# Kernel tuning notes

Measured on AMD Instinct MI355X. Metric: run time of the kernel, lower is better.

## Reference

```python
import jax, jax.numpy as jnp
import numpy as np

L_MAX = 2    # l in {0,1,2}, m-dim sizes 2l+1
NU_MAX = 3   # body order
K = 8        # number of CG m-combinations kept per l_tuple
Q = 16       # radial channels
S = 256      # atomic environments (samples)


def _build_structure():
    """Deterministically build combine_indices + multiplicities (module state).
    Returns {nu: [(l_tuple, idx_prev[K], idx_1[K], mult[K]), ...]} in sorted order."""
    rng = np.random.default_rng(0)
    struct = {}
    # nu = 2: l_tuples are nondecreasing pairs; previous level is LE_1 with m-dim 2*l1+1
    struct[2] = []
    for l1 in range(L_MAX + 1):
        for l2 in range(l1, L_MAX + 1):
            ip = jnp.asarray(rng.integers(0, 2 * l1 + 1, K), dtype=jnp.int32)
            i1 = jnp.asarray(rng.integers(0, 2 * l2 + 1, K), dtype=jnp.int32)
            mult = jnp.asarray((rng.random(K) + 0.5).astype(np.float32))
            struct[2].append(((l1, l2), ip, i1, mult))
    # nu = 3: previous level tensors have m-dim K
    struct[3] = []
    for l1 in range(L_MAX + 1):
        for l2 in range(l1, L_MAX + 1):
            for l3 in range(l2, L_MAX + 1):
                ip = jnp.asarray(rng.integers(0, K, K), dtype=jnp.int32)
                i1 = jnp.asarray(rng.integers(0, 2 * l3 + 1, K), dtype=jnp.int32)
                mult = jnp.asarray((rng.random(K) + 0.5).astype(np.float32))
                struct[3].append(((l1, l2, l3), ip, i1, mult))
    return struct


def setup_inputs() -> dict:
    key = jax.random.key(0)
    k0, k1, k2 = jax.random.split(key, 3)
    return {
        "LE1_l0": jax.random.normal(k0, (1, Q, S), dtype=jnp.float32),
        "LE1_l1": jax.random.normal(k1, (3, Q, S), dtype=jnp.float32),
        "LE1_l2": jax.random.normal(k2, (5, Q, S), dtype=jnp.float32),
    }


def reference(LE1_l0, LE1_l1, LE1_l2):
    struct = _build_structure()
    LE1 = {(0,): LE1_l0, (1,): LE1_l1, (2,): LE1_l2}
    feats = {1: LE1}
    # Build all levels from UNSCALED parents (multiplicities applied afterwards,
    # matching the torch loop order exactly).
    for nu in range(2, NU_MAX + 1):
        cur = {}
        for lt, ip, i1, _ in struct[nu]:
            A = jnp.take(feats[nu - 1][lt[:-1]], ip, axis=0)[:, :, None, :]  # [K, F, 1, S]
            B = jnp.take(LE1[(lt[-1],)], i1, axis=0)[:, None, :, :]          # [K, 1, Q, S]
            cur[lt] = (A * B).reshape(K, -1, S)                               # [K, F*Q, S]
        feats[nu] = cur
    # Apply multiplicities, then flatten everything into one [total_rows, S] output
    outs = []
    for nu in range(2, NU_MAX + 1):
        for lt, _, _, mult in struct[nu]:
            outs.append((feats[nu][lt] * mult[:, None, None]).reshape(-1, S))
    return jnp.concatenate(outs, axis=0)
```

## Files before the change

### kernel.cpp

```cpp
#include <hip/hip_runtime.h>
#include <stdint.h>
#include <stddef.h>

#define KK 8
#define QQ 16
#define SS 256
#define NU2_ROWS 12288u

typedef float f32x4 __attribute__((ext_vector_type(4)));

namespace {

struct NpPcg64 {
  unsigned __int128 state, inc;
  uint32_t uinteger;
  bool has_uint32;

  static unsigned __int128 mul128() {
    return (((unsigned __int128)2549297995355413924ULL) << 64) | 4865540595714422341ULL;
  }
  void step() { state = state * mul128() + inc; }
  uint64_t next64() {
    step();
    uint64_t hi = (uint64_t)(state >> 64), lo = (uint64_t)state;
    uint64_t x = hi ^ lo;
    unsigned rot = (unsigned)(state >> 122) & 63u;
    return (x >> rot) | (x << ((64u - rot) & 63u));
  }
  uint32_t next32() {
    if (has_uint32) { has_uint32 = false; return uinteger; }
    uint64_t n = next64();
    has_uint32 = true;
    uinteger = (uint32_t)(n >> 32);
    return (uint32_t)n;
  }
  double nextd() {
    return (double)(next64() >> 11) * (1.0 / 9007199254740992.0);
  }
  uint32_t lemire32(uint32_t rng) {
    uint32_t excl = rng + 1u;
    uint64_t m = (uint64_t)next32() * (uint64_t)excl;
    uint32_t leftover = (uint32_t)m;
    if (leftover < excl) {
      uint32_t threshold = (uint32_t)((0xFFFFFFFFu - rng) % excl);
      while (leftover < threshold) {
        m = (uint64_t)next32() * (uint64_t)excl;
        leftover = (uint32_t)m;
      }
    }
    return (uint32_t)(m >> 32);
  }
  void integers(int high, int* out, int n) {
    if (high <= 1) { for (int i = 0; i < n; i++) out[i] = 0; return; }
    uint32_t rng = (uint32_t)(high - 1);
    for (int i = 0; i < n; i++) out[i] = (int)lemire32(rng);
  }
  void mults(float* out, int n) {
    for (int i = 0; i < n; i++) out[i] = (float)(nextd() + 0.5);
  }
};

void seed_rng0(NpPcg64& r) {
  uint32_t pool[4];
  uint32_t hc = 0x43b0d7e5u;
  auto hashmix = [&hc](uint32_t v) -> uint32_t {
    v ^= hc; hc *= 0x931e8875u; v *= hc; v ^= v >> 16; return v;
  };
  auto mix = [](uint32_t x, uint32_t y) -> uint32_t {
    uint32_t m = 0xca01f9ddu * x - 0x4973f715u * y; m ^= m >> 16; return m;
  };
  for (int i = 0; i < 4; i++) pool[i] = hashmix(0u);
  for (int is = 0; is < 4; is++)
    for (int id = 0; id < 4; id++)
      if (is != id) pool[id] = mix(pool[id], hashmix(pool[is]));
  uint32_t hb = 0x8b51f9ddu;
  uint32_t w[8];
  for (int i = 0; i < 8; i++) {
    uint32_t v = pool[i & 3];
    v ^= hb; hb *= 0x58f38dedu; v *= hb; v ^= v >> 16;
    w[i] = v;
  }
  uint64_t sd[4];
  for (int i = 0; i < 4; i++) sd[i] = (uint64_t)w[2 * i] | ((uint64_t)w[2 * i + 1] << 32);
  unsigned __int128 initstate = (((unsigned __int128)sd[0]) << 64) | sd[1];
  unsigned __int128 initseq   = (((unsigned __int128)sd[2]) << 64) | sd[3];
  r.state = 0; r.inc = (initseq << 1) | 1;
  r.step(); r.state += initstate; r.step();
  r.has_uint32 = false; r.uinteger = 0;
}

struct Args {
  const float* pA2[6][KK];
  const float* pB2[6][KK];
  float        m2[6][KK];
  const float* pX3[10][KK];
  const float* pY3[10][KK];
  const float* pZ3[10][KK];
  float        m3[10][KK];
};

}

__global__ __launch_bounds__(256) void le_kernel(Args a, float* __restrict__ out) {
  unsigned gwave = (blockIdx.x * 256u + threadIdx.x) >> 6;
  unsigned s4 = (threadIdx.x & 63u) << 2;

  if (gwave < 1280u) {
    unsigned t = gwave >> 7, k = (gwave >> 4) & 7u, q1 = gwave & 15u;
    const f32x4 vx = *(const f32x4*)(a.pX3[t][k] + q1 * SS + s4);
    const float* py = a.pY3[t][k] + s4;
    const float* pz = a.pZ3[t][k] + s4;
    f32x4 vy[16], vz[16];
#pragma unroll
    for (int i = 0; i < 16; i++) vy[i] = *(const f32x4*)(py + i * SS);
#pragma unroll
    for (int i = 0; i < 16; i++) vz[i] = *(const f32x4*)(pz + i * SS);
    float m = a.m3[t][k];
    float* po = out + (size_t)(NU2_ROWS + ((t * 8u + k) * 16u + q1) * 256u) * SS + s4;
#pragma unroll
    for (int q2 = 0; q2 < 16; q2++) {
      f32x4 xy = vx * vy[q2];
      float* pr = po + (size_t)(q2 * 16) * SS;
#pragma unroll
      for (int q3 = 0; q3 < 16; q3++) {
        f32x4 r = (xy * vz[q3]) * m;
        *(f32x4*)(pr + q3 * SS) = r;
      }
    }
  } else {
    unsigned u = gwave - 1280u;
    unsigned t = u >> 7, k = (u >> 4) & 7u, q1 = u & 15u;
    const f32x4 va = *(const f32x4*)(a.pA2[t][k] + q1 * SS + s4);
    const float* pb = a.pB2[t][k] + s4;
    float m = a.m2[t][k];
    float* po = out + (size_t)((t * 8u + k) * 16u + q1) * 16u * SS + s4;
#pragma unroll
    for (int q2 = 0; q2 < 16; q2++) {
      f32x4 vb = *(const f32x4*)(pb + q2 * SS);
      f32x4 r = (va * vb) * m;
      *(f32x4*)(po + q2 * SS) = r;
    }
  }
}

extern "C" void kernel_launch(void* const* d_in, const int* in_sizes, int n_in,
                              void* d_out, int out_size, void* d_ws, size_t ws_size,
                              hipStream_t stream) {
  (void)in_sizes; (void)n_in; (void)d_ws; (void)ws_size; (void)out_size;

  NpPcg64 rng;
  seed_rng0(rng);

  static const int pairs[6][2] = {{0,0},{0,1},{0,2},{1,1},{1,2},{2,2}};
  static const int trip[10][3] = {{0,0,0},{0,0,1},{0,0,2},{0,1,1},{0,1,2},
                                  {0,2,2},{1,1,1},{1,1,2},{1,2,2},{2,2,2}};
  static const int parent[10]  = {0,0,0,1,1,2,3,3,4,5};

  int   ip2[6][KK], i12[6][KK];
  float m2v[6][KK];
  for (int t = 0; t < 6; t++) {
    rng.integers(2 * pairs[t][0] + 1, ip2[t], KK);
    rng.integers(2 * pairs[t][1] + 1, i12[t], KK);
    rng.mults(m2v[t], KK);
  }
  int   ip3[10][KK], i13[10][KK];
  float m3v[10][KK];
  for (int u = 0; u < 10; u++) {
    rng.integers(KK, ip3[u], KK);
    rng.integers(2 * trip[u][2] + 1, i13[u], KK);
    rng.mults(m3v[u], KK);
  }

  const float* base[3] = {(const float*)d_in[0], (const float*)d_in[1], (const float*)d_in[2]};
  Args a;
  for (int t = 0; t < 6; t++) {
    for (int k = 0; k < KK; k++) {
      a.pA2[t][k] = base[pairs[t][0]] + (size_t)ip2[t][k] * QQ * SS;
      a.pB2[t][k] = base[pairs[t][1]] + (size_t)i12[t][k] * QQ * SS;
      a.m2[t][k]  = m2v[t][k];
    }
  }
  for (int u = 0; u < 10; u++) {
    for (int k = 0; k < KK; k++) {
      int p = parent[u], kp = ip3[u][k];
      a.pX3[u][k] = base[pairs[p][0]] + (size_t)ip2[p][kp] * QQ * SS;
      a.pY3[u][k] = base[pairs[p][1]] + (size_t)i12[p][kp] * QQ * SS;
      a.pZ3[u][k] = base[trip[u][2]] + (size_t)i13[u][k] * QQ * SS;
      a.m3[u][k]  = m3v[u][k];
    }
  }

  le_kernel<<<512, 256, 0, stream>>>(a, (float*)d_out);
}
```

Measured before the change: 71.83 us.

## Rebalance work into fine-grained quarter-row units with software-pipelined loads

Replaces the uneven per-wave split, where nu=3 waves wrote 256 rows each and nu=2 waves wrote 16, with uniform work units of 4 output rows. Each wave takes a contiguous, evenly sized range of these units. The next unit's loads are double-buffered so they overlap with the current unit's stores. The launch changes to 256 blocks of 512 threads. This aims to remove load imbalance and tail effects in a store-bound kernel, at the cost of redundant re-loads of the vx/vy/z vectors per unit and more index arithmetic.

```diff
diff --git a/kernel.cpp b/kernel.cpp
--- a/kernel.cpp
+++ b/kernel.cpp
@@ -101,46 +101,66 @@
 
 }
 
-__global__ __launch_bounds__(256) void le_kernel(Args a, float* __restrict__ out) {
-  unsigned gwave = (blockIdx.x * 256u + threadIdx.x) >> 6;
+struct QBuf {
+  f32x4 vx, vy, r0, r1, r2, r3;
+  float m;
+  float* po;
+};
+
+__device__ __forceinline__ void load_q(const Args& a, unsigned qd, unsigned s4,
+                                       float* __restrict__ out, QBuf& b) {
+  unsigned u = qd >> 2, part = qd & 3u;
+  if (u < 768u) {
+    unsigned t = u >> 7, k = (u >> 4) & 7u, q1 = u & 15u;
+    b.vx = *(const f32x4*)(a.pA2[t][k] + q1 * SS + s4);
+    b.vy = (f32x4)(1.0f);
+    const float* pr = a.pB2[t][k] + part * 4u * SS + s4;
+    b.r0 = *(const f32x4*)(pr);
+    b.r1 = *(const f32x4*)(pr + SS);
+    b.r2 = *(const f32x4*)(pr + 2u * SS);
+    b.r3 = *(const f32x4*)(pr + 3u * SS);
+    b.m = a.m2[t][k];
+    b.po = out + (size_t)(((t * 8u + k) * 16u + q1) * 16u + part * 4u) * SS + s4;
+  } else {
+    unsigned v = u - 768u;
+    unsigned t = v >> 11, k = (v >> 8) & 7u, q1 = (v >> 4) & 15u, q2 = v & 15u;
+    b.vx = *(const f32x4*)(a.pX3[t][k] + q1 * SS + s4);
+    b.vy = *(const f32x4*)(a.pY3[t][k] + q2 * SS + s4);
+    const float* pr = a.pZ3[t][k] + part * 4u * SS + s4;
+    b.r0 = *(const f32x4*)(pr);
+    b.r1 = *(const f32x4*)(pr + SS);
+    b.r2 = *(const f32x4*)(pr + 2u * SS);
+    b.r3 = *(const f32x4*)(pr + 3u * SS);
+    b.m = a.m3[t][k];
+    b.po = out + (size_t)(NU2_ROWS +
+                          (((t * 8u + k) * 16u + q1) * 16u + q2) * 16u + part * 4u) * SS + s4;
+  }
+}
+
+__device__ __forceinline__ void proc_q(const QBuf& b) {
+  f32x4 F = b.vx * b.vy;
+  *(f32x4*)(b.po)           = (F * b.r0) * b.m;
+  *(f32x4*)(b.po + SS)      = (F * b.r1) * b.m;
+  *(f32x4*)(b.po + 2u * SS) = (F * b.r2) * b.m;
+  *(f32x4*)(b.po + 3u * SS) = (F * b.r3) * b.m;
+}
+
+__global__ __launch_bounds__(512) void le_kernel(Args a, float* __restrict__ out) {
+  unsigned w = (blockIdx.x * 512u + threadIdx.x) >> 6;
   unsigned s4 = (threadIdx.x & 63u) << 2;
-
-  if (gwave < 1280u) {
-    unsigned t = gwave >> 7, k = (gwave >> 4) & 7u, q1 = gwave & 15u;
-    const f32x4 vx = *(const f32x4*)(a.pX3[t][k] + q1 * SS + s4);
-    const float* py = a.pY3[t][k] + s4;
-    const float* pz = a.pZ3[t][k] + s4;
-    f32x4 vy[16], vz[16];
-#pragma unroll
-    for (int i = 0; i < 16; i++) vy[i] = *(const f32x4*)(py + i * SS);
-#pragma unroll
-    for (int i = 0; i < 16; i++) vz[i] = *(const f32x4*)(pz + i * SS);
-    float m = a.m3[t][k];
-    float* po = out + (size_t)(NU2_ROWS + ((t * 8u + k) * 16u + q1) * 256u) * SS + s4;
-#pragma unroll
-    for (int q2 = 0; q2 < 16; q2++) {
-      f32x4 xy = vx * vy[q2];
-      float* pr = po + (size_t)(q2 * 16) * SS;
-#pragma unroll
-      for (int q3 = 0; q3 < 16; q3++) {
-        f32x4 r = (xy * vz[q3]) * m;
-        *(f32x4*)(pr + q3 * SS) = r;
-      }
-    }
-  } else {
-    unsigned u = gwave - 1280u;
-    unsigned t = u >> 7, k = (u >> 4) & 7u, q1 = u & 15u;
-    const f32x4 va = *(const f32x4*)(a.pA2[t][k] + q1 * SS + s4);
-    const float* pb = a.pB2[t][k] + s4;
-    float m = a.m2[t][k];
-    float* po = out + (size_t)((t * 8u + k) * 16u + q1) * 16u * SS + s4;
-#pragma unroll
-    for (int q2 = 0; q2 < 16; q2++) {
-      f32x4 vb = *(const f32x4*)(pb + q2 * SS);
-      f32x4 r = (va * vb) * m;
-      *(f32x4*)(po + q2 * SS) = r;
-    }
-  }
+  unsigned qs = (w * 83u) >> 1;
+  unsigned n = (((w + 1u) * 83u) >> 1) - qs;
+
+  QBuf A, B;
+  load_q(a, qs, s4, out, A);
+  unsigned j = 0;
+  for (; j + 1u < n; j += 2u) {
+    load_q(a, qs + j + 1u, s4, out, B);
+    proc_q(A);
+    if (j + 2u < n) load_q(a, qs + j + 2u, s4, out, A);
+    proc_q(B);
+  }
+  if (j < n) proc_q(A);
 }
 
 extern "C" void kernel_launch(void* const* d_in, const int* in_sizes, int n_in,
@@ -190,5 +210,5 @@
     }
   }
 
-  le_kernel<<<512, 256, 0, stream>>>(a, (float*)d_out);
-}
+  le_kernel<<<256, 512, 0, stream>>>(a, (float*)d_out);
+}
```

Result: slower. 85.59 us (+19.2%).
